# Performance work log

Hardware: AMD Instinct MI355X
Metric: run time of the kernel (lower is better)

## Reference

```python
import jax, jax.numpy as jnp
import numpy as np

N, E, D, H, L = 50000, 800000, 64, 4, 2
DH = D // H


def layer_norm(h, g, b, eps=1e-5):
    mu = h.mean(-1, keepdims=True)
    var = ((h - mu) ** 2).mean(-1, keepdims=True)
    return (h - mu) / jnp.sqrt(var + eps) * g + b


def setup_inputs() -> dict:
    key = jax.random.key(0)
    ks = jax.random.split(key, 16)
    s = 1.0 / np.sqrt(D)
    inp = {
        "x": jax.random.normal(ks[0], (N, D), jnp.float32),
        "edge_attr": jax.random.normal(ks[1], (E, D), jnp.float32),
        "edge_index": jax.random.randint(ks[2], (2, E), 0, N, jnp.int64),
        "WQ": jax.random.normal(ks[3], (L, D, D), jnp.float32) * s,
        "WK": jax.random.normal(ks[4], (L, D, D), jnp.float32) * s,
        "WE": jax.random.normal(ks[5], (L, D, D), jnp.float32) * s,
        "WV": jax.random.normal(ks[6], (L, D, D), jnp.float32) * s,
        "WO": jax.random.normal(ks[7], (L, D, D), jnp.float32) * s,
        "bO": jnp.zeros((L, D), jnp.float32),
        "ln1_g": jnp.ones((L, D), jnp.float32),
        "ln1_b": jnp.zeros((L, D), jnp.float32),
        "W1": jax.random.normal(ks[8], (L, D, 2 * D), jnp.float32) * s,
        "b1": jnp.zeros((L, 2 * D), jnp.float32),
        "W2": jax.random.normal(ks[9], (L, 2 * D, D), jnp.float32) * (1.0 / np.sqrt(2 * D)),
        "b2": jnp.zeros((L, D), jnp.float32),
        "ln2_g": jnp.ones((L, D), jnp.float32),
        "ln2_b": jnp.zeros((L, D), jnp.float32),
    }
    return inp


def exphormer_layer(h, edge_attr, src, dst, p):
    (wq, wk, we, wv, wo, bo, g1, be1, w1, b1, w2, b2, g2, be2) = p
    n = h.shape[0]
    Qh = (h @ wq).reshape(n, H, DH)
    Kh = (h @ wk).reshape(n, H, DH)
    Vh = (h @ wv).reshape(n, H, DH)
    Eh = (edge_attr @ we).reshape(-1, H, DH)
    # per-edge score: sum over head_dim of K[src]*Q[dst]*E / sqrt(DH)
    s = jnp.sum(Kh[src] * Qh[dst] * Eh, axis=-1, keepdims=True) / np.sqrt(DH)
    score = jnp.exp(jnp.clip(s, -5.0, 5.0))  # [E, H, 1]
    msg = Vh[src] * score                     # [E, H, DH]
    wV = jax.ops.segment_sum(msg, dst, num_segments=n)    # [N, H, DH]
    Z = jax.ops.segment_sum(score, dst, num_segments=n)   # [N, H, 1]
    h_attn = (wV / (Z + 1e-6)).reshape(n, D)
    h1 = layer_norm(h + (h_attn @ wo + bo), g1, be1)
    ffn = jax.nn.relu(h1 @ w1 + b1) @ w2 + b2
    return layer_norm(h1 + ffn, g2, be2)


def reference(x, edge_attr, edge_index, WQ, WK, WE, WV, WO, bO, ln1_g, ln1_b,
              W1, b1, W2, b2, ln2_g, ln2_b):
    src = edge_index[0]
    dst = edge_index[1]
    h = x
    for l in range(L):
        p = (WQ[l], WK[l], WE[l], WV[l], WO[l], bO[l], ln1_g[l], ln1_b[l],
             W1[l], b1[l], W2[l], b2[l], ln2_g[l], ln2_b[l])
        h = exphormer_layer(h, edge_attr, src, dst, p)
    return h
```

## Files before the change

### kernel.cpp

```cpp
#include <hip/hip_runtime.h>

#define NN 50000
#define NE 800000
#define D  64
#define NL 2

typedef __bf16 bf16x8 __attribute__((ext_vector_type(8)));
typedef float  floatx4 __attribute__((ext_vector_type(4)));

static __device__ __forceinline__ float bf2f(unsigned short u) {
    return __uint_as_float(((unsigned)u) << 16);
}
static __device__ __forceinline__ unsigned short f2bf(float x) {
    unsigned u = __float_as_uint(x);
    u += 0x7fff + ((u >> 16) & 1);
    return (unsigned short)(u >> 16);
}


__global__ void k_deg(const int* __restrict__ ei, int* __restrict__ deg) {
    int e = blockIdx.x * 256 + threadIdx.x;
    if (e < NE) atomicAdd(&deg[ei[NE + e]], 1);
}

__global__ void k_scan(const int* __restrict__ deg, int* __restrict__ row_off,
                       int* __restrict__ cursor) {
    __shared__ int buf[1024];
    __shared__ int carry_s;
    if (threadIdx.x == 0) carry_s = 0;
    __syncthreads();
    for (int base = 0; base < NN; base += 1024) {
        int i = base + (int)threadIdx.x;
        int v = (i < NN) ? deg[i] : 0;
        buf[threadIdx.x] = v;
        __syncthreads();
        for (int offt = 1; offt < 1024; offt <<= 1) {
            int t = (threadIdx.x >= (unsigned)offt) ? buf[threadIdx.x - offt] : 0;
            __syncthreads();
            buf[threadIdx.x] += t;
            __syncthreads();
        }
        int inc = buf[threadIdx.x] + carry_s;
        if (i < NN) {
            row_off[i + 1] = inc;
            cursor[i] = inc - v;
            if (i == 0) row_off[0] = 0;
        }
        __syncthreads();
        if (threadIdx.x == 1023) carry_s = inc;
        __syncthreads();
    }
}

__global__ void k_scatter(const int* __restrict__ ei, int* __restrict__ cursor,
                          int* __restrict__ csr_src, int* __restrict__ eperm) {
    int e = blockIdx.x * 256 + threadIdx.x;
    if (e < NE) {
        int dst = ei[NE + e];
        int pos = atomicAdd(&cursor[dst], 1);
        csr_src[pos] = ei[e];
        eperm[e] = pos;
    }
}

__global__ __launch_bounds__(256) void k_prep(
        const float* __restrict__ WQ, const float* __restrict__ WK,
        const float* __restrict__ WV, const float* __restrict__ WE,
        const float* __restrict__ WO, const float* __restrict__ W1,
        const float* __restrict__ W2,
        unsigned short* __restrict__ wqT, unsigned short* __restrict__ wkT,
        unsigned short* __restrict__ wvT, unsigned short* __restrict__ weT,
        unsigned short* __restrict__ woT, unsigned short* __restrict__ w1T,
        unsigned short* __restrict__ w2T) {
    int idx = blockIdx.x * 256 + threadIdx.x;
    if (idx >= 2 * 36864) return;
    int l = idx / 36864;
    int r = idx % 36864;
    if (r < 20480) {
        int which = r >> 12, rr = r & 4095;
        int m = rr >> 6, k = rr & 63;
        const float* src = (which == 0 ? WQ : which == 1 ? WK : which == 2 ? WV :
                            which == 3 ? WE : WO);
        unsigned short* dst = (which == 0 ? wqT : which == 1 ? wkT : which == 2 ? wvT :
                               which == 3 ? weT : woT);
        dst[l * 4096 + rr] = f2bf(src[l * 4096 + k * 64 + m]);
    } else if (r < 28672) {
        int r2 = r - 20480;
        int m = r2 >> 6, k = r2 & 63;
        w1T[l * 8192 + r2] = f2bf(W1[l * 8192 + k * 128 + m]);
    } else {
        int r3 = r - 28672;
        int m = r3 >> 7, k = r3 & 127;
        w2T[l * 8192 + r3] = f2bf(W2[l * 8192 + k * 64 + m]);
    }
}


__global__ __launch_bounds__(256) void k_qkv_mfma(const float* __restrict__ h,
        const unsigned short* __restrict__ wqT, const unsigned short* __restrict__ wkT,
        const unsigned short* __restrict__ wvT,
        float* __restrict__ Qh, unsigned short* __restrict__ Kb,
        unsigned short* __restrict__ Vb) {
    __shared__ unsigned short st[4][16 * 72];
    const int lane = threadIdx.x & 63;
    const int w    = threadIdx.x >> 6;
    const int ml   = lane & 15;
    const int quad = lane >> 4;

    bf16x8 aq[2][4], ak[2][4], av[2][4];
#pragma unroll
    for (int kt = 0; kt < 2; kt++)
#pragma unroll
        for (int mt = 0; mt < 4; mt++) {
            int o = (mt*16 + ml)*64 + kt*32 + quad*8;
            aq[kt][mt] = *(const bf16x8*)&wqT[o];
            ak[kt][mt] = *(const bf16x8*)&wkT[o];
            av[kt][mt] = *(const bf16x8*)&wvT[o];
        }

    const int wave = blockIdx.x * 4 + w;
    const int nw   = gridDim.x * 4;
    for (int tile = wave; tile < NN / 16; tile += nw) {
        const int e0 = tile * 16;
        const float4* ar = (const float4*)(h + (size_t)(e0 + ml) * D);
        bf16x8 b[2];
#pragma unroll
        for (int kt = 0; kt < 2; kt++) {
            float4 f0 = ar[kt*8 + quad*2 + 0];
            float4 f1 = ar[kt*8 + quad*2 + 1];
            b[kt][0] = (__bf16)f0.x; b[kt][1] = (__bf16)f0.y;
            b[kt][2] = (__bf16)f0.z; b[kt][3] = (__bf16)f0.w;
            b[kt][4] = (__bf16)f1.x; b[kt][5] = (__bf16)f1.y;
            b[kt][6] = (__bf16)f1.z; b[kt][7] = (__bf16)f1.w;
        }
        floatx4 accq[4] = {}, acck[4] = {}, accv[4] = {};
#pragma unroll
        for (int kt = 0; kt < 2; kt++)
#pragma unroll
            for (int mt = 0; mt < 4; mt++) {
                accq[mt] = __builtin_amdgcn_mfma_f32_16x16x32_bf16(aq[kt][mt], b[kt], accq[mt], 0, 0, 0);
                acck[mt] = __builtin_amdgcn_mfma_f32_16x16x32_bf16(ak[kt][mt], b[kt], acck[mt], 0, 0, 0);
                accv[mt] = __builtin_amdgcn_mfma_f32_16x16x32_bf16(av[kt][mt], b[kt], accv[mt], 0, 0, 0);
            }
#pragma unroll
        for (int mt = 0; mt < 4; mt++)
            *(float4*)(Qh + (size_t)(e0 + ml) * D + mt*16 + quad*4) =
                make_float4(accq[mt][0], accq[mt][1], accq[mt][2], accq[mt][3]);
        const int el = lane >> 2, c = lane & 3;
#pragma unroll
        for (int mt = 0; mt < 4; mt++)
            *(ushort4*)&st[w][ml*72 + mt*16 + quad*4] =
                make_ushort4(f2bf(acck[mt][0]), f2bf(acck[mt][1]),
                             f2bf(acck[mt][2]), f2bf(acck[mt][3]));
        {
            uint4 r0 = *(const uint4*)&st[w][el*72 + c*16 + 0];
            uint4 r1 = *(const uint4*)&st[w][el*72 + c*16 + 8];
            uint4* gp = (uint4*)(Kb + (size_t)(e0 + el) * D + c*16);
            gp[0] = r0; gp[1] = r1;
        }
#pragma unroll
        for (int mt = 0; mt < 4; mt++)
            *(ushort4*)&st[w][ml*72 + mt*16 + quad*4] =
                make_ushort4(f2bf(accv[mt][0]), f2bf(accv[mt][1]),
                             f2bf(accv[mt][2]), f2bf(accv[mt][3]));
        {
            uint4 r0 = *(const uint4*)&st[w][el*72 + c*16 + 0];
            uint4 r1 = *(const uint4*)&st[w][el*72 + c*16 + 8];
            uint4* gp = (uint4*)(Vb + (size_t)(e0 + el) * D + c*16);
            gp[0] = r0; gp[1] = r1;
        }
    }
}

__global__ __launch_bounds__(256) void k_eh_mfma(const float* __restrict__ ea,
        const unsigned short* __restrict__ weT, const int* __restrict__ eperm,
        unsigned short* __restrict__ Eh) {
    __shared__ unsigned short st[4][16 * 72];
    const int lane = threadIdx.x & 63;
    const int w    = threadIdx.x >> 6;
    const int ml   = lane & 15;
    const int quad = lane >> 4;

    bf16x8 afr[2][2][4];
#pragma unroll
    for (int l = 0; l < 2; l++)
#pragma unroll
        for (int kt = 0; kt < 2; kt++)
#pragma unroll
            for (int mt = 0; mt < 4; mt++)
                afr[l][kt][mt] = *(const bf16x8*)&weT[l*4096 + (mt*16 + ml)*64 + kt*32 + quad*8];

    const int wave = blockIdx.x * 4 + w;
    const int nw   = gridDim.x * 4;
    const int el = lane >> 2, c = lane & 3;
    for (int tile = wave; tile < NE / 16; tile += nw) {
        const int e0 = tile * 16;
        const float4* ar = (const float4*)(ea + (size_t)(e0 + ml) * D);
        bf16x8 b[2];
#pragma unroll
        for (int kt = 0; kt < 2; kt++) {
            float4 f0 = ar[kt*8 + quad*2 + 0];
            float4 f1 = ar[kt*8 + quad*2 + 1];
            b[kt][0] = (__bf16)f0.x; b[kt][1] = (__bf16)f0.y;
            b[kt][2] = (__bf16)f0.z; b[kt][3] = (__bf16)f0.w;
            b[kt][4] = (__bf16)f1.x; b[kt][5] = (__bf16)f1.y;
            b[kt][6] = (__bf16)f1.z; b[kt][7] = (__bf16)f1.w;
        }
        int pos = eperm[e0 + el];
#pragma unroll
        for (int l = 0; l < 2; l++) {
            floatx4 acc[4] = {};
#pragma unroll
            for (int kt = 0; kt < 2; kt++)
#pragma unroll
                for (int mt = 0; mt < 4; mt++)
                    acc[mt] = __builtin_amdgcn_mfma_f32_16x16x32_bf16(afr[l][kt][mt], b[kt], acc[mt], 0, 0, 0);
#pragma unroll
            for (int mt = 0; mt < 4; mt++)
                *(ushort4*)&st[w][ml*72 + mt*16 + quad*4] =
                    make_ushort4(f2bf(acc[mt][0]), f2bf(acc[mt][1]),
                                 f2bf(acc[mt][2]), f2bf(acc[mt][3]));
            uint4 r0 = *(const uint4*)&st[w][el*72 + c*16 + 0];
            uint4 r1 = *(const uint4*)&st[w][el*72 + c*16 + 8];
            uint4* gp = (uint4*)(Eh + (size_t)l * NE * D + (size_t)pos * D + c*16);
            gp[0] = r0;
            gp[1] = r1;
        }
    }
}

__global__ __launch_bounds__(256) void k_agg(const float* __restrict__ Qh,
        const unsigned short* __restrict__ Kb, const unsigned short* __restrict__ Vb,
        const unsigned short* __restrict__ Eh,
        const int* __restrict__ row_off, const int* __restrict__ csr_src,
        float* __restrict__ h_attn) {
    const int node = blockIdx.x * 4 + (threadIdx.x >> 6);
    if (node >= NN) return;
    const int lane  = threadIdx.x & 63;
    const int eslot = lane >> 4;
    const int ml    = lane & 15;
    const int beg = row_off[node], end = row_off[node + 1];
    const float4 q = ((const float4*)(Qh + (size_t)node * D))[ml];
    float4 acc = make_float4(0.f, 0.f, 0.f, 0.f);
    float z = 0.f;

    int i0 = beg + eslot;
    while (i0 < end) {
        int i1 = i0 + 4;
        bool a1 = i1 < end;
        int s0 = csr_src[i0];
        int p1 = a1 ? i1 : i0;
        int s1 = a1 ? csr_src[p1] : s0;
        ushort4 kb0 = *(const ushort4*)(Kb + (size_t)s0 * D + ml * 4);
        ushort4 eb0 = *(const ushort4*)(Eh + (size_t)i0 * D + ml * 4);
        ushort4 vb0 = *(const ushort4*)(Vb + (size_t)s0 * D + ml * 4);
        ushort4 kb1 = *(const ushort4*)(Kb + (size_t)s1 * D + ml * 4);
        ushort4 eb1 = *(const ushort4*)(Eh + (size_t)p1 * D + ml * 4);
        ushort4 vb1 = *(const ushort4*)(Vb + (size_t)s1 * D + ml * 4);

        float part0 = bf2f(kb0.x) * q.x * bf2f(eb0.x) + bf2f(kb0.y) * q.y * bf2f(eb0.y)
                    + bf2f(kb0.z) * q.z * bf2f(eb0.z) + bf2f(kb0.w) * q.w * bf2f(eb0.w);
        float part1 = bf2f(kb1.x) * q.x * bf2f(eb1.x) + bf2f(kb1.y) * q.y * bf2f(eb1.y)
                    + bf2f(kb1.z) * q.z * bf2f(eb1.z) + bf2f(kb1.w) * q.w * bf2f(eb1.w);
        part0 += __shfl_xor(part0, 1, 64);
        part0 += __shfl_xor(part0, 2, 64);
        part1 += __shfl_xor(part1, 1, 64);
        part1 += __shfl_xor(part1, 2, 64);
        float sc0 = __expf(fminf(5.f, fmaxf(-5.f, part0 * 0.25f)));
        float sc1 = a1 ? __expf(fminf(5.f, fmaxf(-5.f, part1 * 0.25f))) : 0.f;

        acc.x += sc0 * bf2f(vb0.x) + sc1 * bf2f(vb1.x);
        acc.y += sc0 * bf2f(vb0.y) + sc1 * bf2f(vb1.y);
        acc.z += sc0 * bf2f(vb0.z) + sc1 * bf2f(vb1.z);
        acc.w += sc0 * bf2f(vb0.w) + sc1 * bf2f(vb1.w);
        z += sc0 + sc1;
        i0 += 8;
    }
#pragma unroll
    for (int m = 16; m <= 32; m <<= 1) {
        acc.x += __shfl_xor(acc.x, m, 64);
        acc.y += __shfl_xor(acc.y, m, 64);
        acc.z += __shfl_xor(acc.z, m, 64);
        acc.w += __shfl_xor(acc.w, m, 64);
        z     += __shfl_xor(z, m, 64);
    }
    if (eslot == 0) {
        float inv = 1.f / (z + 1e-6f);
        ((float4*)(h_attn + (size_t)node * D))[ml] =
            make_float4(acc.x * inv, acc.y * inv, acc.z * inv, acc.w * inv);
    }
}

__global__ __launch_bounds__(512) void k_post_mfma(const float* __restrict__ h_in,
        const float* __restrict__ h_attn,
        const unsigned short* __restrict__ woT_g,
        const unsigned short* __restrict__ w1T_g,
        const unsigned short* __restrict__ w2T_g,
        const float* __restrict__ bo,
        const float* __restrict__ g1, const float* __restrict__ be1,
        const float* __restrict__ b1, const float* __restrict__ b2,
        const float* __restrict__ g2, const float* __restrict__ be2,
        float* __restrict__ h_out) {
    __shared__ unsigned short woT_s[64 * 72];
    __shared__ unsigned short w1T_s[128 * 72];
    __shared__ unsigned short w2T_s[64 * 136];
    __shared__ unsigned short stg[8][16 * 136];

    const int t = threadIdx.x;
    {
        const uint4* s0 = (const uint4*)woT_g;
        { int i = t; if (i < 512) { int row = i >> 3, c = i & 7;
              *(uint4*)&woT_s[row*72 + c*8] = s0[i]; } }
        const uint4* s1 = (const uint4*)w1T_g;
        for (int i = t; i < 1024; i += 512) {
            int row = i >> 3, c = i & 7;
            *(uint4*)&w1T_s[row*72 + c*8] = s1[i];
        }
        const uint4* s2 = (const uint4*)w2T_g;
        for (int i = t; i < 1024; i += 512) {
            int row = i >> 4, c = i & 15;
            *(uint4*)&w2T_s[row*136 + c*8] = s2[i];
        }
    }
    __syncthreads();

    const int w = t >> 6, lane = t & 63;
    const int ml = lane & 15, quad = lane >> 4;
    const int tile = blockIdx.x * 8 + w;
    if (tile >= NN / 16) return;
    const int e0 = tile * 16;
    unsigned short* st = stg[w];

    const float4* ap = (const float4*)(h_attn + (size_t)(e0 + ml) * D);
    floatx4 acc1[4] = {};
#pragma unroll
    for (int kt = 0; kt < 2; kt++) {
        float4 f0 = ap[kt*8 + quad*2 + 0];
        float4 f1 = ap[kt*8 + quad*2 + 1];
        bf16x8 b;
        b[0] = (__bf16)f0.x; b[1] = (__bf16)f0.y; b[2] = (__bf16)f0.z; b[3] = (__bf16)f0.w;
        b[4] = (__bf16)f1.x; b[5] = (__bf16)f1.y; b[6] = (__bf16)f1.z; b[7] = (__bf16)f1.w;
#pragma unroll
        for (int mt = 0; mt < 4; mt++) {
            bf16x8 a = *(const bf16x8*)&woT_s[(mt*16 + ml)*72 + kt*32 + quad*8];
            acc1[mt] = __builtin_amdgcn_mfma_f32_16x16x32_bf16(a, b, acc1[mt], 0, 0, 0);
        }
    }
    const float4* hp  = (const float4*)(h_in + (size_t)(e0 + ml) * D);
    const float4* bo4 = (const float4*)bo;
    floatx4 tt[4];
#pragma unroll
    for (int mt = 0; mt < 4; mt++) {
        float4 hh = hp[mt*4 + quad];
        float4 bb = bo4[mt*4 + quad];
        tt[mt][0] = acc1[mt][0] + hh.x + bb.x;
        tt[mt][1] = acc1[mt][1] + hh.y + bb.y;
        tt[mt][2] = acc1[mt][2] + hh.z + bb.z;
        tt[mt][3] = acc1[mt][3] + hh.w + bb.w;
    }
    float s = 0.f;
#pragma unroll
    for (int mt = 0; mt < 4; mt++) s += tt[mt][0] + tt[mt][1] + tt[mt][2] + tt[mt][3];
    s += __shfl_xor(s, 16, 64); s += __shfl_xor(s, 32, 64);
    float mu = s * (1.f / 64.f);
    float v = 0.f;
#pragma unroll
    for (int mt = 0; mt < 4; mt++)
#pragma unroll
        for (int r = 0; r < 4; r++) { float c = tt[mt][r] - mu; v += c * c; }
    v += __shfl_xor(v, 16, 64); v += __shfl_xor(v, 32, 64);
    float rstd = rsqrtf(v * (1.f / 64.f) + 1e-5f);
    const float4* g1v  = (const float4*)g1;
    const float4* be1v = (const float4*)be1;
    floatx4 h1[4];
#pragma unroll
    for (int mt = 0; mt < 4; mt++) {
        float4 gg = g1v[mt*4 + quad];
        float4 bb = be1v[mt*4 + quad];
        h1[mt][0] = (tt[mt][0] - mu) * rstd * gg.x + bb.x;
        h1[mt][1] = (tt[mt][1] - mu) * rstd * gg.y + bb.y;
        h1[mt][2] = (tt[mt][2] - mu) * rstd * gg.z + bb.z;
        h1[mt][3] = (tt[mt][3] - mu) * rstd * gg.w + bb.w;
        *(ushort4*)&st[ml*136 + mt*16 + quad*4] =
            make_ushort4(f2bf(h1[mt][0]), f2bf(h1[mt][1]), f2bf(h1[mt][2]), f2bf(h1[mt][3]));
    }

    bf16x8 bh[2];
#pragma unroll
    for (int kt = 0; kt < 2; kt++)
        bh[kt] = *(const bf16x8*)&st[ml*136 + kt*32 + quad*8];
    floatx4 acc2[8] = {};
#pragma unroll
    for (int kt = 0; kt < 2; kt++)
#pragma unroll
        for (int mt = 0; mt < 8; mt++) {
            bf16x8 a = *(const bf16x8*)&w1T_s[(mt*16 + ml)*72 + kt*32 + quad*8];
            acc2[mt] = __builtin_amdgcn_mfma_f32_16x16x32_bf16(a, bh[kt], acc2[mt], 0, 0, 0);
        }
    const float4* b1v = (const float4*)b1;
#pragma unroll
    for (int mt = 0; mt < 8; mt++) {
        float4 bb = b1v[mt*4 + quad];
        float y0 = fmaxf(acc2[mt][0] + bb.x, 0.f);
        float y1 = fmaxf(acc2[mt][1] + bb.y, 0.f);
        float y2 = fmaxf(acc2[mt][2] + bb.z, 0.f);
        float y3 = fmaxf(acc2[mt][3] + bb.w, 0.f);
        *(ushort4*)&st[ml*136 + mt*16 + quad*4] =
            make_ushort4(f2bf(y0), f2bf(y1), f2bf(y2), f2bf(y3));
    }

    floatx4 acc3[4] = {};
#pragma unroll
    for (int kt = 0; kt < 4; kt++) {
        bf16x8 b = *(const bf16x8*)&st[ml*136 + kt*32 + quad*8];
#pragma unroll
        for (int mt = 0; mt < 4; mt++) {
            bf16x8 a = *(const bf16x8*)&w2T_s[(mt*16 + ml)*136 + kt*32 + quad*8];
            acc3[mt] = __builtin_amdgcn_mfma_f32_16x16x32_bf16(a, b, acc3[mt], 0, 0, 0);
        }
    }
    const float4* b2v = (const float4*)b2;
#pragma unroll
    for (int mt = 0; mt < 4; mt++) {
        float4 bb = b2v[mt*4 + quad];
        tt[mt][0] = acc3[mt][0] + bb.x + h1[mt][0];
        tt[mt][1] = acc3[mt][1] + bb.y + h1[mt][1];
        tt[mt][2] = acc3[mt][2] + bb.z + h1[mt][2];
        tt[mt][3] = acc3[mt][3] + bb.w + h1[mt][3];
    }
    s = 0.f;
#pragma unroll
    for (int mt = 0; mt < 4; mt++) s += tt[mt][0] + tt[mt][1] + tt[mt][2] + tt[mt][3];
    s += __shfl_xor(s, 16, 64); s += __shfl_xor(s, 32, 64);
    mu = s * (1.f / 64.f);
    v = 0.f;
#pragma unroll
    for (int mt = 0; mt < 4; mt++)
#pragma unroll
        for (int r = 0; r < 4; r++) { float c = tt[mt][r] - mu; v += c * c; }
    v += __shfl_xor(v, 16, 64); v += __shfl_xor(v, 32, 64);
    rstd = rsqrtf(v * (1.f / 64.f) + 1e-5f);
    const float4* g2v  = (const float4*)g2;
    const float4* be2v = (const float4*)be2;
    float4* outp = (float4*)(h_out + (size_t)(e0 + ml) * D);
#pragma unroll
    for (int mt = 0; mt < 4; mt++) {
        float4 gg = g2v[mt*4 + quad];
        float4 bb = be2v[mt*4 + quad];
        float4 o;
        o.x = (tt[mt][0] - mu) * rstd * gg.x + bb.x;
        o.y = (tt[mt][1] - mu) * rstd * gg.y + bb.y;
        o.z = (tt[mt][2] - mu) * rstd * gg.z + bb.z;
        o.w = (tt[mt][3] - mu) * rstd * gg.w + bb.w;
        outp[mt*4 + quad] = o;
    }
}


extern "C" void kernel_launch(void* const* d_in, const int* in_sizes, int n_in,
                              void* d_out, int out_size, void* d_ws, size_t ws_size,
                              hipStream_t stream) {
    const float* x   = (const float*)d_in[0];
    const float* ea  = (const float*)d_in[1];
    const int*   ei  = (const int*)d_in[2];
    const float* WQ  = (const float*)d_in[3];
    const float* WK  = (const float*)d_in[4];
    const float* WE  = (const float*)d_in[5];
    const float* WV  = (const float*)d_in[6];
    const float* WO  = (const float*)d_in[7];
    const float* bO  = (const float*)d_in[8];
    const float* g1  = (const float*)d_in[9];
    const float* be1 = (const float*)d_in[10];
    const float* W1  = (const float*)d_in[11];
    const float* b1  = (const float*)d_in[12];
    const float* W2  = (const float*)d_in[13];
    const float* b2  = (const float*)d_in[14];
    const float* g2  = (const float*)d_in[15];
    const float* be2 = (const float*)d_in[16];
    float* out = (float*)d_out;

    char* wsb = (char*)d_ws;
    size_t off = 0;
    auto alloc = [&](size_t bytes) {
        void* p = wsb + off;
        off += (bytes + 255) & ~(size_t)255;
        return p;
    };
    float* Qh            = (float*)alloc((size_t)NN * D * 4);
    unsigned short* Kb   = (unsigned short*)alloc((size_t)NN * D * 2);
    unsigned short* Vb   = (unsigned short*)alloc((size_t)NN * D * 2);
    float* hbuf          = (float*)alloc((size_t)NN * D * 4);
    float* hattn         = (float*)alloc((size_t)NN * D * 4);
    unsigned short* Eh   = (unsigned short*)alloc((size_t)NL * NE * D * 2);
    int* row_off         = (int*)alloc((size_t)(NN + 1) * 4);
    int* cursor          = (int*)alloc((size_t)NN * 4);
    int* deg             = (int*)alloc((size_t)NN * 4);
    int* csr_src         = (int*)alloc((size_t)NE * 4);
    int* eperm           = (int*)alloc((size_t)NE * 4);
    unsigned short* wqT  = (unsigned short*)alloc((size_t)2 * 4096 * 2);
    unsigned short* wkT  = (unsigned short*)alloc((size_t)2 * 4096 * 2);
    unsigned short* wvT  = (unsigned short*)alloc((size_t)2 * 4096 * 2);
    unsigned short* weT  = (unsigned short*)alloc((size_t)2 * 4096 * 2);
    unsigned short* woT  = (unsigned short*)alloc((size_t)2 * 4096 * 2);
    unsigned short* w1T  = (unsigned short*)alloc((size_t)2 * 8192 * 2);
    unsigned short* w2T  = (unsigned short*)alloc((size_t)2 * 8192 * 2);

    hipMemsetAsync(deg, 0, (size_t)NN * 4, stream);
    k_deg<<<(NE + 255) / 256, 256, 0, stream>>>(ei, deg);
    k_scan<<<1, 1024, 0, stream>>>(deg, row_off, cursor);
    k_scatter<<<(NE + 255) / 256, 256, 0, stream>>>(ei, cursor, csr_src, eperm);
    k_prep<<<(2 * 36864 + 255) / 256, 256, 0, stream>>>(WQ, WK, WV, WE, WO, W1, W2,
            wqT, wkT, wvT, weT, woT, w1T, w2T);
    k_eh_mfma<<<1024, 256, 0, stream>>>(ea, weT, eperm, Eh);

    for (int l = 0; l < NL; l++) {
        const float* hcur = (l == 0) ? x : hbuf;
        float* hnxt = (l == NL - 1) ? out : hbuf;
        k_qkv_mfma<<<782, 256, 0, stream>>>(hcur, wqT + l * 4096, wkT + l * 4096,
                                            wvT + l * 4096, Qh, Kb, Vb);
        k_agg<<<(NN + 3) / 4, 256, 0, stream>>>(Qh, Kb, Vb, Eh + (size_t)l * NE * D,
                                                row_off, csr_src, hattn);
        k_post_mfma<<<(NN / 16 + 7) / 8, 512, 0, stream>>>(hcur, hattn,
                woT + l * 4096, w1T + l * 8192, w2T + l * 8192,
                bO + l * 64, g1 + l * 64, be1 + l * 64,
                b1 + l * 128, b2 + l * 64,
                g2 + l * 64, be2 + l * 64, hnxt);
    }
}
```

Before: 717.7 us.

## Compute edge scores inside the edge projection kernel instead of materializing Eh

Removes the stored bf16 per-edge projection Eh (about 200MB across both layers) and adds a per-layer k_score kernel. It recomputes edge_attr@WE with MFMA, gathers K[src] and Q[dst], and writes only the four per-head clipped exp scores in CSR order. The aggregation kernel then reads just those scores plus V, and Q is stored as bf16 rather than fp32. The scan also becomes a chunked two-level scan instead of a serial 1024-wide block loop. The trade-off is that the edge_attr GEMM runs again in each layer and K/Q are gathered randomly per edge in edge order.

```diff
diff --git a/kernel.cpp b/kernel.cpp
--- a/kernel.cpp
+++ b/kernel.cpp
@@ -23,32 +23,29 @@
     if (e < NE) atomicAdd(&deg[ei[NE + e]], 1);
 }
 
-__global__ void k_scan(const int* __restrict__ deg, int* __restrict__ row_off,
-                       int* __restrict__ cursor) {
-    __shared__ int buf[1024];
-    __shared__ int carry_s;
-    if (threadIdx.x == 0) carry_s = 0;
+__global__ __launch_bounds__(1024) void k_scan(const int* __restrict__ deg,
+        int* __restrict__ row_off, int* __restrict__ cursor) {
+    __shared__ int sums[1024];
+    const int t = threadIdx.x;
+    const int CH = (NN + 1023) / 1024;
+    int b = t * CH, e = b + CH; if (e > NN) e = NN; if (b > NN) b = NN;
+    int s = 0;
+    for (int i = b; i < e; i++) s += deg[i];
+    sums[t] = s;
     __syncthreads();
-    for (int base = 0; base < NN; base += 1024) {
-        int i = base + (int)threadIdx.x;
-        int v = (i < NN) ? deg[i] : 0;
-        buf[threadIdx.x] = v;
+    for (int off = 1; off < 1024; off <<= 1) {
+        int v = (t >= off) ? sums[t - off] : 0;
         __syncthreads();
-        for (int offt = 1; offt < 1024; offt <<= 1) {
-            int t = (threadIdx.x >= (unsigned)offt) ? buf[threadIdx.x - offt] : 0;
-            __syncthreads();
-            buf[threadIdx.x] += t;
-            __syncthreads();
-        }
-        int inc = buf[threadIdx.x] + carry_s;
-        if (i < NN) {
-            row_off[i + 1] = inc;
-            cursor[i] = inc - v;
-            if (i == 0) row_off[0] = 0;
-        }
+        sums[t] += v;
         __syncthreads();
-        if (threadIdx.x == 1023) carry_s = inc;
-        __syncthreads();
+    }
+    int run = sums[t] - s;
+    if (t == 0) row_off[0] = 0;
+    for (int i = b; i < e; i++) {
+        int d = deg[i];
+        cursor[i] = run;
+        run += d;
+        row_off[i + 1] = run;
     }
 }
 
@@ -99,7 +96,7 @@
 __global__ __launch_bounds__(256) void k_qkv_mfma(const float* __restrict__ h,
         const unsigned short* __restrict__ wqT, const unsigned short* __restrict__ wkT,
         const unsigned short* __restrict__ wvT,
-        float* __restrict__ Qh, unsigned short* __restrict__ Kb,
+        unsigned short* __restrict__ Qb, unsigned short* __restrict__ Kb,
         unsigned short* __restrict__ Vb) {
     __shared__ unsigned short st[4][16 * 72];
     const int lane = threadIdx.x & 63;
@@ -120,6 +117,7 @@
 
     const int wave = blockIdx.x * 4 + w;
     const int nw   = gridDim.x * 4;
+    const int el = lane >> 2, c = lane & 3;
     for (int tile = wave; tile < NN / 16; tile += nw) {
         const int e0 = tile * 16;
         const float4* ar = (const float4*)(h + (size_t)(e0 + ml) * D);
@@ -142,57 +140,43 @@
                 acck[mt] = __builtin_amdgcn_mfma_f32_16x16x32_bf16(ak[kt][mt], b[kt], acck[mt], 0, 0, 0);
                 accv[mt] = __builtin_amdgcn_mfma_f32_16x16x32_bf16(av[kt][mt], b[kt], accv[mt], 0, 0, 0);
             }
-#pragma unroll
-        for (int mt = 0; mt < 4; mt++)
-            *(float4*)(Qh + (size_t)(e0 + ml) * D + mt*16 + quad*4) =
-                make_float4(accq[mt][0], accq[mt][1], accq[mt][2], accq[mt][3]);
-        const int el = lane >> 2, c = lane & 3;
-#pragma unroll
-        for (int mt = 0; mt < 4; mt++)
-            *(ushort4*)&st[w][ml*72 + mt*16 + quad*4] =
-                make_ushort4(f2bf(acck[mt][0]), f2bf(acck[mt][1]),
-                             f2bf(acck[mt][2]), f2bf(acck[mt][3]));
-        {
+        unsigned short* outs[3] = {Qb, Kb, Vb};
+        floatx4* accs[3] = {accq, acck, accv};
+#pragma unroll
+        for (int m = 0; m < 3; m++) {
+            floatx4* a = accs[m];
+#pragma unroll
+            for (int mt = 0; mt < 4; mt++)
+                *(ushort4*)&st[w][ml*72 + mt*16 + quad*4] =
+                    make_ushort4(f2bf(a[mt][0]), f2bf(a[mt][1]),
+                                 f2bf(a[mt][2]), f2bf(a[mt][3]));
             uint4 r0 = *(const uint4*)&st[w][el*72 + c*16 + 0];
             uint4 r1 = *(const uint4*)&st[w][el*72 + c*16 + 8];
-            uint4* gp = (uint4*)(Kb + (size_t)(e0 + el) * D + c*16);
+            uint4* gp = (uint4*)(outs[m] + (size_t)(e0 + el) * D + c*16);
             gp[0] = r0; gp[1] = r1;
         }
-#pragma unroll
-        for (int mt = 0; mt < 4; mt++)
-            *(ushort4*)&st[w][ml*72 + mt*16 + quad*4] =
-                make_ushort4(f2bf(accv[mt][0]), f2bf(accv[mt][1]),
-                             f2bf(accv[mt][2]), f2bf(accv[mt][3]));
-        {
-            uint4 r0 = *(const uint4*)&st[w][el*72 + c*16 + 0];
-            uint4 r1 = *(const uint4*)&st[w][el*72 + c*16 + 8];
-            uint4* gp = (uint4*)(Vb + (size_t)(e0 + el) * D + c*16);
-            gp[0] = r0; gp[1] = r1;
-        }
-    }
-}
-
-__global__ __launch_bounds__(256) void k_eh_mfma(const float* __restrict__ ea,
-        const unsigned short* __restrict__ weT, const int* __restrict__ eperm,
-        unsigned short* __restrict__ Eh) {
-    __shared__ unsigned short st[4][16 * 72];
+    }
+}
+
+__global__ __launch_bounds__(256) void k_score(const float* __restrict__ ea,
+        const unsigned short* __restrict__ weT, const int* __restrict__ ei,
+        const int* __restrict__ eperm,
+        const unsigned short* __restrict__ Qb, const unsigned short* __restrict__ Kb,
+        float* __restrict__ sc_out) {
     const int lane = threadIdx.x & 63;
     const int w    = threadIdx.x >> 6;
     const int ml   = lane & 15;
     const int quad = lane >> 4;
 
-    bf16x8 afr[2][2][4];
-#pragma unroll
-    for (int l = 0; l < 2; l++)
-#pragma unroll
-        for (int kt = 0; kt < 2; kt++)
-#pragma unroll
-            for (int mt = 0; mt < 4; mt++)
-                afr[l][kt][mt] = *(const bf16x8*)&weT[l*4096 + (mt*16 + ml)*64 + kt*32 + quad*8];
+    bf16x8 afr[2][4];
+#pragma unroll
+    for (int kt = 0; kt < 2; kt++)
+#pragma unroll
+        for (int mt = 0; mt < 4; mt++)
+            afr[kt][mt] = *(const bf16x8*)&weT[(mt*16 + ml)*64 + kt*32 + quad*8];
 
     const int wave = blockIdx.x * 4 + w;
     const int nw   = gridDim.x * 4;
-    const int el = lane >> 2, c = lane & 3;
     for (int tile = wave; tile < NE / 16; tile += nw) {
         const int e0 = tile * 16;
         const float4* ar = (const float4*)(ea + (size_t)(e0 + ml) * D);
@@ -206,32 +190,37 @@
             b[kt][4] = (__bf16)f1.x; b[kt][5] = (__bf16)f1.y;
             b[kt][6] = (__bf16)f1.z; b[kt][7] = (__bf16)f1.w;
         }
-        int pos = eperm[e0 + el];
-#pragma unroll
-        for (int l = 0; l < 2; l++) {
-            floatx4 acc[4] = {};
-#pragma unroll
-            for (int kt = 0; kt < 2; kt++)
-#pragma unroll
-                for (int mt = 0; mt < 4; mt++)
-                    acc[mt] = __builtin_amdgcn_mfma_f32_16x16x32_bf16(afr[l][kt][mt], b[kt], acc[mt], 0, 0, 0);
+        int s_e = ei[e0 + ml];
+        int d_e = ei[NE + e0 + ml];
+        floatx4 acc[4] = {};
+#pragma unroll
+        for (int kt = 0; kt < 2; kt++)
 #pragma unroll
             for (int mt = 0; mt < 4; mt++)
-                *(ushort4*)&st[w][ml*72 + mt*16 + quad*4] =
-                    make_ushort4(f2bf(acc[mt][0]), f2bf(acc[mt][1]),
-                                 f2bf(acc[mt][2]), f2bf(acc[mt][3]));
-            uint4 r0 = *(const uint4*)&st[w][el*72 + c*16 + 0];
-            uint4 r1 = *(const uint4*)&st[w][el*72 + c*16 + 8];
-            uint4* gp = (uint4*)(Eh + (size_t)l * NE * D + (size_t)pos * D + c*16);
-            gp[0] = r0;
-            gp[1] = r1;
-        }
-    }
-}
-
-__global__ __launch_bounds__(256) void k_agg(const float* __restrict__ Qh,
-        const unsigned short* __restrict__ Kb, const unsigned short* __restrict__ Vb,
-        const unsigned short* __restrict__ Eh,
+                acc[mt] = __builtin_amdgcn_mfma_f32_16x16x32_bf16(afr[kt][mt], b[kt], acc[mt], 0, 0, 0);
+        float sc4[4];
+#pragma unroll
+        for (int mt = 0; mt < 4; mt++) {
+            ushort4 kk = *(const ushort4*)(Kb + (size_t)s_e * D + mt*16 + quad*4);
+            ushort4 qq = *(const ushort4*)(Qb + (size_t)d_e * D + mt*16 + quad*4);
+            float p = acc[mt][0] * bf2f(kk.x) * bf2f(qq.x)
+                    + acc[mt][1] * bf2f(kk.y) * bf2f(qq.y)
+                    + acc[mt][2] * bf2f(kk.z) * bf2f(qq.z)
+                    + acc[mt][3] * bf2f(kk.w) * bf2f(qq.w);
+            p += __shfl_xor(p, 16, 64);
+            p += __shfl_xor(p, 32, 64);
+            sc4[mt] = __expf(fminf(5.f, fmaxf(-5.f, p * 0.25f)));
+        }
+        if (quad == 0) {
+            int pos = eperm[e0 + ml];
+            *(float4*)(sc_out + (size_t)pos * 4) =
+                make_float4(sc4[0], sc4[1], sc4[2], sc4[3]);
+        }
+    }
+}
+
+__global__ __launch_bounds__(256) void k_agg(const unsigned short* __restrict__ Vb,
+        const float* __restrict__ sc,
         const int* __restrict__ row_off, const int* __restrict__ csr_src,
         float* __restrict__ h_attn) {
     const int node = blockIdx.x * 4 + (threadIdx.x >> 6);
@@ -239,42 +228,26 @@
     const int lane  = threadIdx.x & 63;
     const int eslot = lane >> 4;
     const int ml    = lane & 15;
+    const int head  = ml >> 2;
     const int beg = row_off[node], end = row_off[node + 1];
-    const float4 q = ((const float4*)(Qh + (size_t)node * D))[ml];
     float4 acc = make_float4(0.f, 0.f, 0.f, 0.f);
     float z = 0.f;
 
-    int i0 = beg + eslot;
-    while (i0 < end) {
+    for (int i0 = beg + eslot; i0 < end; i0 += 8) {
         int i1 = i0 + 4;
         bool a1 = i1 < end;
-        int s0 = csr_src[i0];
         int p1 = a1 ? i1 : i0;
-        int s1 = a1 ? csr_src[p1] : s0;
-        ushort4 kb0 = *(const ushort4*)(Kb + (size_t)s0 * D + ml * 4);
-        ushort4 eb0 = *(const ushort4*)(Eh + (size_t)i0 * D + ml * 4);
-        ushort4 vb0 = *(const ushort4*)(Vb + (size_t)s0 * D + ml * 4);
-        ushort4 kb1 = *(const ushort4*)(Kb + (size_t)s1 * D + ml * 4);
-        ushort4 eb1 = *(const ushort4*)(Eh + (size_t)p1 * D + ml * 4);
-        ushort4 vb1 = *(const ushort4*)(Vb + (size_t)s1 * D + ml * 4);
-
-        float part0 = bf2f(kb0.x) * q.x * bf2f(eb0.x) + bf2f(kb0.y) * q.y * bf2f(eb0.y)
-                    + bf2f(kb0.z) * q.z * bf2f(eb0.z) + bf2f(kb0.w) * q.w * bf2f(eb0.w);
-        float part1 = bf2f(kb1.x) * q.x * bf2f(eb1.x) + bf2f(kb1.y) * q.y * bf2f(eb1.y)
-                    + bf2f(kb1.z) * q.z * bf2f(eb1.z) + bf2f(kb1.w) * q.w * bf2f(eb1.w);
-        part0 += __shfl_xor(part0, 1, 64);
-        part0 += __shfl_xor(part0, 2, 64);
-        part1 += __shfl_xor(part1, 1, 64);
-        part1 += __shfl_xor(part1, 2, 64);
-        float sc0 = __expf(fminf(5.f, fmaxf(-5.f, part0 * 0.25f)));
-        float sc1 = a1 ? __expf(fminf(5.f, fmaxf(-5.f, part1 * 0.25f))) : 0.f;
-
-        acc.x += sc0 * bf2f(vb0.x) + sc1 * bf2f(vb1.x);
-        acc.y += sc0 * bf2f(vb0.y) + sc1 * bf2f(vb1.y);
-        acc.z += sc0 * bf2f(vb0.z) + sc1 * bf2f(vb1.z);
-        acc.w += sc0 * bf2f(vb0.w) + sc1 * bf2f(vb1.w);
-        z += sc0 + sc1;
-        i0 += 8;
+        float s0 = sc[(size_t)i0 * 4 + head];
+        float s1 = a1 ? sc[(size_t)p1 * 4 + head] : 0.f;
+        int v0 = csr_src[i0];
+        int v1 = csr_src[p1];
+        ushort4 vb0 = *(const ushort4*)(Vb + (size_t)v0 * D + ml * 4);
+        ushort4 vb1 = *(const ushort4*)(Vb + (size_t)v1 * D + ml * 4);
+        acc.x += s0 * bf2f(vb0.x) + s1 * bf2f(vb1.x);
+        acc.y += s0 * bf2f(vb0.y) + s1 * bf2f(vb1.y);
+        acc.z += s0 * bf2f(vb0.z) + s1 * bf2f(vb1.z);
+        acc.w += s0 * bf2f(vb0.w) + s1 * bf2f(vb1.w);
+        z += s0 + s1;
     }
 #pragma unroll
     for (int m = 16; m <= 32; m <<= 1) {
@@ -486,12 +459,12 @@
         off += (bytes + 255) & ~(size_t)255;
         return p;
     };
-    float* Qh            = (float*)alloc((size_t)NN * D * 4);
+    unsigned short* Qb   = (unsigned short*)alloc((size_t)NN * D * 2);
     unsigned short* Kb   = (unsigned short*)alloc((size_t)NN * D * 2);
     unsigned short* Vb   = (unsigned short*)alloc((size_t)NN * D * 2);
     float* hbuf          = (float*)alloc((size_t)NN * D * 4);
     float* hattn         = (float*)alloc((size_t)NN * D * 4);
-    unsigned short* Eh   = (unsigned short*)alloc((size_t)NL * NE * D * 2);
+    float* scb           = (float*)alloc((size_t)NE * 4 * 4);
     int* row_off         = (int*)alloc((size_t)(NN + 1) * 4);
     int* cursor          = (int*)alloc((size_t)NN * 4);
     int* deg             = (int*)alloc((size_t)NN * 4);
@@ -511,15 +484,14 @@
     k_scatter<<<(NE + 255) / 256, 256, 0, stream>>>(ei, cursor, csr_src, eperm);
     k_prep<<<(2 * 36864 + 255) / 256, 256, 0, stream>>>(WQ, WK, WV, WE, WO, W1, W2,
             wqT, wkT, wvT, weT, woT, w1T, w2T);
-    k_eh_mfma<<<1024, 256, 0, stream>>>(ea, weT, eperm, Eh);
 
     for (int l = 0; l < NL; l++) {
         const float* hcur = (l == 0) ? x : hbuf;
         float* hnxt = (l == NL - 1) ? out : hbuf;
         k_qkv_mfma<<<782, 256, 0, stream>>>(hcur, wqT + l * 4096, wkT + l * 4096,
-                                            wvT + l * 4096, Qh, Kb, Vb);
-        k_agg<<<(NN + 3) / 4, 256, 0, stream>>>(Qh, Kb, Vb, Eh + (size_t)l * NE * D,
-                                                row_off, csr_src, hattn);
+                                            wvT + l * 4096, Qb, Kb, Vb);
+        k_score<<<1024, 256, 0, stream>>>(ea, weT + l * 4096, ei, eperm, Qb, Kb, scb);
+        k_agg<<<(NN + 3) / 4, 256, 0, stream>>>(Vb, scb, row_off, csr_src, hattn);
         k_post_mfma<<<(NN / 16 + 7) / 8, 512, 0, stream>>>(hcur, hattn,
                 woT + l * 4096, w1T + l * 8192, w2T + l * 8192,
                 bO + l * 64, g1 + l * 64, be1 + l * 64,
```

Result: slower. 740.5 us (+3.2%).
